# Kernel optimization log

Hardware: AMD Instinct MI355X
Metric: run time of the kernel (lower is better)

## Reference

```python
import jax, jax.numpy as jnp
import numpy as np

B, H, W, C = 32, 56, 56, 192
WS, SS, NH = 7, 3, 6  # window, shift, heads
N = WS * WS
HIDDEN = int(C * 4.0)
TABLE = (2 * WS - 1) * (2 * WS - 1)  # 169
EPS = 1e-5

# Relative position index, faithful to the source (meshgrid default 'xy',
# and the source multiplies BOTH coord channels by (2*ws-1), so indices can
# exceed the table size; gather uses clip like jnp.take's jit behavior).
_coords = np.stack(np.meshgrid(np.arange(WS), np.arange(WS))).reshape(2, -1)
_rel = (_coords[:, :, None] - _coords[:, None, :]).transpose(1, 2, 0)
_rel = (_rel + WS - 1) * (2 * WS - 1)
REL_IDX = jnp.asarray(_rel.sum(-1))  # [N, N]

# Shift attention mask (static), labels regions then marks cross-region pairs.
_m = np.zeros((H, W))
_cnt = 0
for hs in [slice(0, -WS), slice(-WS, -SS), slice(-SS, None)]:
    for ws_ in [slice(0, -WS), slice(-WS, -SS), slice(-SS, None)]:
        _m[hs, ws_] = _cnt
        _cnt += 1
_mw = _m.reshape(H // WS, WS, W // WS, WS).transpose(0, 2, 1, 3).reshape(-1, N)
ATTN_MASK = jnp.asarray((_mw[:, None, :] != _mw[:, :, None]).astype(np.float32))  # [nW, N, N]
NW = ATTN_MASK.shape[0]


def layer_norm(x, g, b):
    mu = jnp.mean(x, axis=-1, keepdims=True)
    xc = x - mu
    var = jnp.mean(xc * xc, axis=-1, keepdims=True)
    return xc * jax.lax.rsqrt(var + EPS) * g + b


def window_partition(x):  # [B,H,W,C] -> [B*nW, N, C]
    x = x.reshape(B, H // WS, WS, W // WS, WS, C).transpose(0, 1, 3, 2, 4, 5)
    return x.reshape(-1, N, C)


def window_reverse(w):  # [B*nW, N, C] -> [B,H,W,C]
    x = w.reshape(B, H // WS, W // WS, WS, WS, C).transpose(0, 1, 3, 2, 4, 5)
    return x.reshape(B, H, W, C)


def setup_inputs() -> dict:
    key = jax.random.key(0)
    ks = jax.random.split(key, 16)
    s = lambda fan_in: 1.0 / np.sqrt(fan_in)
    return {
        "x": jax.random.normal(ks[0], (B, H * W, C), jnp.float32),
        "norm1_g": jnp.ones((C,), jnp.float32),
        "norm1_b": jnp.zeros((C,), jnp.float32),
        "qkv_w": jax.random.normal(ks[1], (C, 3 * C), jnp.float32) * s(C),
        "qkv_b": jnp.zeros((3 * C,), jnp.float32),
        "rel_table": jax.random.normal(ks[2], (TABLE, NH), jnp.float32) * 0.02,
        "proj_w": jax.random.normal(ks[3], (C, C), jnp.float32) * s(C),
        "proj_b": jnp.zeros((C,), jnp.float32),
        "norm2_g": jnp.ones((C,), jnp.float32),
        "norm2_b": jnp.zeros((C,), jnp.float32),
        "fc1_w": jax.random.normal(ks[4], (C, HIDDEN), jnp.float32) * s(C),
        "fc1_b": jnp.zeros((HIDDEN,), jnp.float32),
        "fc2_w": jax.random.normal(ks[5], (HIDDEN, C), jnp.float32) * s(HIDDEN),
        "fc2_b": jnp.zeros((C,), jnp.float32),
    }


def reference(x, norm1_g, norm1_b, qkv_w, qkv_b, rel_table, proj_w, proj_b,
              norm2_g, norm2_b, fc1_w, fc1_b, fc2_w, fc2_b):
    shortcut = x
    h = layer_norm(x, norm1_g, norm1_b).reshape(B, H, W, C)
    # cyclic shift
    h = jnp.roll(h, shift=(-SS, -SS), axis=(1, 2))
    xw = window_partition(h)  # [B*nW, N, C]

    # window attention
    qkv = xw @ qkv_w + qkv_b  # [B*nW, N, 3C]
    q, k, v = jnp.split(qkv, 3, axis=-1)
    hd = C // NH
    q = q.reshape(-1, N, NH, hd).transpose(0, 2, 1, 3) * (hd ** -0.5)
    k = k.reshape(-1, N, NH, hd).transpose(0, 2, 1, 3)
    v = v.reshape(-1, N, NH, hd).transpose(0, 2, 1, 3)
    attn = jnp.einsum("whnd,whmd->whnm", q, k)  # [B*nW, NH, N, N]
    bias = jnp.take(rel_table, REL_IDX, axis=0, mode="clip")  # [N,N,NH]
    attn = attn + bias.transpose(2, 0, 1)[None]
    attn = attn.reshape(B, NW, NH, N, N) + ATTN_MASK[None, :, None] * -100.0
    attn = jax.nn.softmax(attn.reshape(-1, NH, N, N), axis=-1)
    o = jnp.einsum("whnm,whmd->whnd", attn, v)
    o = o.transpose(0, 2, 1, 3).reshape(-1, N, C)
    o = o @ proj_w + proj_b

    h = window_reverse(o)
    h = jnp.roll(h, shift=(SS, SS), axis=(1, 2)).reshape(B, H * W, C)
    x = shortcut + h
    # MLP
    m = layer_norm(x, norm2_g, norm2_b)
    m = jax.nn.gelu(m @ fc1_w + fc1_b, approximate=False) @ fc2_w + fc2_b
    return x + m
```

## Files before the change

### kernel.cpp

```cpp
#include <hip/hip_runtime.h>
#include <hip/hip_bf16.h>


using f32x4  = __attribute__((ext_vector_type(4))) float;
using short8 = __attribute__((ext_vector_type(8))) short;
typedef unsigned short ushort_t;

__device__ __forceinline__ ushort_t f2bf(float f) {
    __hip_bfloat16 h = __float2bfloat16(f);
    return __builtin_bit_cast(ushort_t, h);
}
__device__ __forceinline__ f32x4 mfma16(short8 a, short8 b, f32x4 c) {
    return __builtin_amdgcn_mfma_f32_16x16x32_bf16(a, b, c, 0, 0, 0);
}
__device__ __forceinline__ float fast_gelu(float h) {
    float hh = h * h;
    float p  = __builtin_fmaf(hh, 0.044715f, 1.0f);
    float z  = h * (-1.5957691216057308f);
    float em = __expf(p * z);
    return h * __builtin_amdgcn_rcpf(1.0f + em);
}

#define CC 192

#define OFF_QKVT   0
#define OFF_PROJT  221184
#define OFF_FC1T   294912
#define OFF_FC2T   589824
#define OFF_BIAS   884736
#define OFF_MASK   942592
#define OFF_BMT    1557504
#define OFF_QG     7848960
#define OFF_KG     46384128
#define OFF_VG     84919296
#define WS_NEED    123454464
#define PREP_SMALL 610438
#define PREP_BIG   2183302

__global__ void prep_kernel(const float* __restrict__ qkv_w, const float* __restrict__ proj_w,
                            const float* __restrict__ fc1_w, const float* __restrict__ fc2_w,
                            const float* __restrict__ rel_table,
                            ushort_t* __restrict__ qkvT, ushort_t* __restrict__ projT,
                            ushort_t* __restrict__ fc1T, ushort_t* __restrict__ fc2T,
                            float* __restrict__ biasT, float* __restrict__ maskT,
                            float* __restrict__ bmT, int full) {
    int idx = blockIdx.x * 256 + threadIdx.x;
    if (idx < 110592) { int n = idx / 192, k = idx % 192; qkvT[idx] = f2bf(qkv_w[k * 576 + n]); return; }
    idx -= 110592;
    if (idx < 36864) { int n = idx / 192, k = idx % 192; projT[idx] = f2bf(proj_w[k * 192 + n]); return; }
    idx -= 36864;
    if (idx < 147456) { int n = idx / 192, k = idx % 192; fc1T[idx] = f2bf(fc1_w[k * 768 + n]); return; }
    idx -= 147456;
    if (idx < 147456) { int n = idx / 768, k = idx % 768; fc2T[idx] = f2bf(fc2_w[k * 192 + n]); return; }
    idx -= 147456;
    if (idx < 14406) {
        int h = idx / 2401; int rest = idx % 2401; int a = rest / 49, b = rest % 49;
        int d = 13 * ((a % 7) - (b % 7) + (a / 7) - (b / 7) + 12);
        if (d > 168) d = 168;
        biasT[idx] = rel_table[d * 6 + h];
        return;
    }
    idx -= 14406;
    if (idx < 153664) {
        int w = idx / 2401; int rest = idx % 2401; int a = rest / 49, b = rest % 49;
        int wy = w / 8, wx = w % 8;
        int ya = wy * 7 + a / 7, xa = wx * 7 + a % 7;
        int yb = wy * 7 + b / 7, xb = wx * 7 + b % 7;
        int lya = ya < 49 ? 0 : (ya < 53 ? 1 : 2);
        int lxa = xa < 49 ? 0 : (xa < 53 ? 1 : 2);
        int lyb = yb < 49 ? 0 : (yb < 53 ? 1 : 2);
        int lxb = xb < 49 ? 0 : (xb < 53 ? 1 : 2);
        maskT[idx] = ((lya * 3 + lxa) != (lyb * 3 + lxb)) ? -100.0f : 0.0f;
        return;
    }
    idx -= 153664;
    if (full && idx < 1572864) {
        int wi = idx / 24576; int r2 = idx % 24576;
        int h = r2 / 4096; int r3 = r2 % 4096;
        int col = r3 / 64, row = r3 % 64;
        float v = -1e30f;
        if (row < 49 && col < 49) {
            int d = 13 * ((row % 7) - (col % 7) + (row / 7) - (col / 7) + 12);
            if (d > 168) d = 168;
            float bias = rel_table[d * 6 + h];
            int wy = wi / 8, wx = wi % 8;
            int ya = wy * 7 + row / 7, xa = wx * 7 + row % 7;
            int yb = wy * 7 + col / 7, xb = wx * 7 + col % 7;
            int lya = ya < 49 ? 0 : (ya < 53 ? 1 : 2);
            int lxa = xa < 49 ? 0 : (xa < 53 ? 1 : 2);
            int lyb = yb < 49 ? 0 : (yb < 53 ? 1 : 2);
            int lxb = xb < 49 ? 0 : (xb < 53 ? 1 : 2);
            float mask = ((lya * 3 + lxa) != (lyb * 3 + lxb)) ? -100.0f : 0.0f;
            v = bias + mask;
        }
        bmT[idx] = v;
        return;
    }
}

__global__ __launch_bounds__(256, 3) void lnqkv_kernel(
    const float* __restrict__ x, const float* __restrict__ n1g, const float* __restrict__ n1b,
    const ushort_t* __restrict__ qkvT, const float* __restrict__ qkv_b,
    ushort_t* __restrict__ qg, ushort_t* __restrict__ kg, ushort_t* __restrict__ vg) {
    __shared__ ushort_t xln [64 * 200];
    __shared__ ushort_t qkvs[64 * 200];
    const int tid = threadIdx.x;
    const int wave = tid >> 6, lane = tid & 63;
    const int ln16 = lane & 15, sub = lane >> 4;
    const int t0 = blockIdx.x * 64;
    const f32x4 zero4 = {0.f, 0.f, 0.f, 0.f};

    {
        float g0 = n1g[lane], g1 = n1g[lane + 64], g2 = n1g[lane + 128];
        float bb0 = n1b[lane], bb1 = n1b[lane + 64], bb2 = n1b[lane + 128];
        for (int rb = 0; rb < 4; ++rb) {
            int row0 = wave * 16 + rb * 4;
            float v0[4], v1[4], v2[4], s[4], q[4];
            #pragma unroll
            for (int j = 0; j < 4; ++j) {
                const float* xr = x + (size_t)(t0 + row0 + j) * CC;
                v0[j] = xr[lane]; v1[j] = xr[lane + 64]; v2[j] = xr[lane + 128];
            }
            #pragma unroll
            for (int j = 0; j < 4; ++j) {
                s[j] = v0[j] + v1[j] + v2[j];
                q[j] = v0[j] * v0[j] + v1[j] * v1[j] + v2[j] * v2[j];
            }
            #pragma unroll
            for (int m = 32; m; m >>= 1) {
                #pragma unroll
                for (int j = 0; j < 4; ++j) { s[j] += __shfl_xor(s[j], m); q[j] += __shfl_xor(q[j], m); }
            }
            #pragma unroll
            for (int j = 0; j < 4; ++j) {
                float mu = s[j] * (1.0f / 192.0f);
                float var = q[j] * (1.0f / 192.0f) - mu * mu;
                float rs = rsqrtf(var + 1e-5f);
                int row = row0 + j;
                xln[row * 200 + lane]       = f2bf((v0[j] - mu) * rs * g0 + bb0);
                xln[row * 200 + lane + 64]  = f2bf((v1[j] - mu) * rs * g1 + bb1);
                xln[row * 200 + lane + 128] = f2bf((v2[j] - mu) * rs * g2 + bb2);
            }
        }
    }
    __syncthreads();

    ushort_t* dsts[3] = {qg, kg, vg};
    for (int v = 0; v < 3; ++v) {
        f32x4 acc[4][3];
        #pragma unroll
        for (int m = 0; m < 4; ++m)
            #pragma unroll
            for (int n = 0; n < 3; ++n) acc[m][n] = zero4;
        for (int kk = 0; kk < 6; ++kk) {
            short8 a[4];
            #pragma unroll
            for (int m = 0; m < 4; ++m)
                a[m] = *(const short8*)(xln + (m * 16 + ln16) * 200 + kk * 32 + 8 * sub);
            #pragma unroll
            for (int n = 0; n < 3; ++n) {
                short8 b = *(const short8*)(qkvT + (size_t)(v * 192 + (wave * 3 + n) * 16 + ln16) * 192 + kk * 32 + 8 * sub);
                #pragma unroll
                for (int m = 0; m < 4; ++m) acc[m][n] = mfma16(a[m], b, acc[m][n]);
            }
        }
        #pragma unroll
        for (int n = 0; n < 3; ++n) {
            int col = (wave * 3 + n) * 16 + ln16;
            float bv = qkv_b[v * 192 + col];
            #pragma unroll
            for (int m = 0; m < 4; ++m)
                #pragma unroll
                for (int r = 0; r < 4; ++r) {
                    int row = m * 16 + 4 * sub + r;
                    float val = acc[m][n][r] + bv;
                    if (v == 0) val *= 0.17677669529663689f;
                    qkvs[row * 200 + col] = f2bf(val);
                }
        }
        __syncthreads();
        ushort_t* dst = dsts[v];
        for (int i = tid; i < 1536; i += 256) {
            int row = i / 24, c = i % 24;
            short8 vv = *(const short8*)(qkvs + row * 200 + c * 8);
            *(short8*)(dst + (size_t)(t0 + row) * 192 + c * 8) = vv;
        }
        __syncthreads();
    }
}

__global__ __launch_bounds__(256, 4) void attnwin_kernel(
    const float* __restrict__ x, const float* __restrict__ proj_b,
    const ushort_t* __restrict__ qg, const ushort_t* __restrict__ kg,
    const ushort_t* __restrict__ vg, const ushort_t* __restrict__ projT,
    const float* __restrict__ bmT, float* __restrict__ out) {
    __shared__ ushort_t vt[192 * 72];
    __shared__ ushort_t PO[4][16 * 72];
    const int tid = threadIdx.x;
    const int wave = tid >> 6, lane = tid & 63;
    const int ln16 = lane & 15, sub = lane >> 4;
    const int win = blockIdx.x;
    const int b = win >> 6, wi = win & 63;
    const int wy = wi >> 3, wx = wi & 7;
    const f32x4 zero4 = {0.f, 0.f, 0.f, 0.f};

    {
        int j = tid & 63;
        int jj = j < 49 ? j : 48;
        int y  = wy * 7 + jj / 7 + 3; if (y >= 56) y -= 56;
        int xx = wx * 7 + jj % 7 + 3; if (xx >= 56) xx -= 56;
        size_t tokV = (size_t)(b * 3136 + y * 56 + xx);
        const bool valid = j < 49;
        #pragma unroll
        for (int pass = 0; pass < 6; ++pass) {
            int c8 = pass * 32 + (tid >> 6) * 8;
            if (valid) {
                short8 vv = *(const short8*)(vg + tokV * 192 + c8);
                #pragma unroll
                for (int q = 0; q < 8; ++q) vt[(c8 + q) * 72 + j] = ((ushort_t*)&vv)[q];
            } else {
                #pragma unroll
                for (int q = 0; q < 8; ++q) vt[(c8 + q) * 72 + j] = 0;
            }
        }
    }

    size_t tokA;
    {
        int j = wave * 16 + ln16; if (j > 48) j = 48;
        int y  = wy * 7 + j / 7 + 3; if (y >= 56) y -= 56;
        int xx = wx * 7 + j % 7 + 3; if (xx >= 56) xx -= 56;
        tokA = (size_t)(b * 3136 + y * 56 + xx);
    }
    size_t tokB[4];
    #pragma unroll
    for (int n = 0; n < 4; ++n) {
        int j = n * 16 + ln16; if (j > 48) j = 48;
        int y  = wy * 7 + j / 7 + 3; if (y >= 56) y -= 56;
        int xx = wx * 7 + j % 7 + 3; if (xx >= 56) xx -= 56;
        tokB[n] = (size_t)(b * 3136 + y * 56 + xx);
    }

    f32x4 accP[12];
    #pragma unroll
    for (int n = 0; n < 12; ++n) accP[n] = zero4;

    ushort_t* Pw = PO[wave];
    const float* bmw = bmT + (size_t)wi * 24576 + (size_t)(wave * 16 + 4 * sub);
    __syncthreads();

    for (int h = 0; h < 6; ++h) {
        short8 qf = *(const short8*)(qg + tokA * 192 + h * 32 + 8 * sub);
        f32x4 s4[4];
        #pragma unroll
        for (int n = 0; n < 4; ++n) {
            short8 kf = *(const short8*)(kg + tokB[n] * 192 + h * 32 + 8 * sub);
            s4[n] = mfma16(qf, kf, zero4);
        }
        #pragma unroll
        for (int n = 0; n < 4; ++n) {
            int col = n * 16 + ln16;
            f32x4 bv = *(const f32x4*)(bmw + h * 4096 + col * 64);
            #pragma unroll
            for (int r = 0; r < 4; ++r) s4[n][r] += bv[r];
        }
        #pragma unroll
        for (int r = 0; r < 4; ++r) {
            float mx = fmaxf(fmaxf(s4[0][r], s4[1][r]), fmaxf(s4[2][r], s4[3][r]));
            mx = fmaxf(mx, __shfl_xor(mx, 1, 16));
            mx = fmaxf(mx, __shfl_xor(mx, 2, 16));
            mx = fmaxf(mx, __shfl_xor(mx, 4, 16));
            mx = fmaxf(mx, __shfl_xor(mx, 8, 16));
            float e0 = __expf(s4[0][r] - mx), e1 = __expf(s4[1][r] - mx);
            float e2 = __expf(s4[2][r] - mx), e3 = __expf(s4[3][r] - mx);
            float sm = e0 + e1 + e2 + e3;
            sm += __shfl_xor(sm, 1, 16);
            sm += __shfl_xor(sm, 2, 16);
            sm += __shfl_xor(sm, 4, 16);
            sm += __shfl_xor(sm, 8, 16);
            float inv = 1.0f / sm;
            int rl = 4 * sub + r;
            Pw[rl * 72 +      ln16] = f2bf(e0 * inv);
            Pw[rl * 72 + 16 + ln16] = f2bf(e1 * inv);
            Pw[rl * 72 + 32 + ln16] = f2bf(e2 * inv);
            Pw[rl * 72 + 48 + ln16] = f2bf(e3 * inv);
        }
        short8 ap0 = *(const short8*)(Pw + ln16 * 72 + 8 * sub);
        short8 ap1 = *(const short8*)(Pw + ln16 * 72 + 32 + 8 * sub);
        f32x4 o2[2]; o2[0] = zero4; o2[1] = zero4;
        #pragma unroll
        for (int n2 = 0; n2 < 2; ++n2) {
            short8 bv0 = *(const short8*)(vt + (h * 32 + n2 * 16 + ln16) * 72 + 8 * sub);
            short8 bv1 = *(const short8*)(vt + (h * 32 + n2 * 16 + ln16) * 72 + 32 + 8 * sub);
            o2[n2] = mfma16(ap0, bv0, o2[n2]);
            o2[n2] = mfma16(ap1, bv1, o2[n2]);
        }
        #pragma unroll
        for (int n2 = 0; n2 < 2; ++n2)
            #pragma unroll
            for (int r = 0; r < 4; ++r)
                Pw[(4 * sub + r) * 72 + n2 * 16 + ln16] = f2bf(o2[n2][r]);
        {
            short8 ao = *(const short8*)(Pw + ln16 * 72 + 8 * sub);
            #pragma unroll
            for (int n = 0; n < 12; ++n) {
                short8 bp = *(const short8*)(projT + (size_t)(n * 16 + ln16) * 192 + h * 32 + 8 * sub);
                accP[n] = mfma16(ao, bp, accP[n]);
            }
        }
    }

    #pragma unroll
    for (int n = 0; n < 12; ++n) {
        int col = n * 16 + ln16;
        float pb = proj_b[col];
        #pragma unroll
        for (int r = 0; r < 4; ++r) {
            int row = wave * 16 + 4 * sub + r;
            if (row < 49) {
                int y  = wy * 7 + row / 7 + 3; if (y >= 56) y -= 56;
                int xx = wx * 7 + row % 7 + 3; if (xx >= 56) xx -= 56;
                size_t g = (size_t)(b * 3136 + y * 56 + xx) * CC;
                out[g + col] = accP[n][r] + pb + x[g + col];
            }
        }
    }
}

__global__ __launch_bounds__(256, 3) void attn_kernel(
    const float* __restrict__ x, const float* __restrict__ n1g, const float* __restrict__ n1b,
    const float* __restrict__ qkv_b, const float* __restrict__ proj_b,
    const ushort_t* __restrict__ qkvT, const ushort_t* __restrict__ projT,
    const float* __restrict__ biasT, const float* __restrict__ maskT,
    float* __restrict__ out) {
    __shared__ ushort_t xln[64 * 200];
    __shared__ ushort_t qo [64 * 40];
    __shared__ ushort_t kl [64 * 40];
    __shared__ ushort_t vt [32 * 72];
    __shared__ ushort_t Pl [64 * 72];
    const int tid = threadIdx.x;
    const int wave = tid >> 6, lane = tid & 63;
    const int ln16 = lane & 15, sub = lane >> 4;
    const int w = blockIdx.x;
    const int batch = w >> 6, wi = w & 63;
    const int wy = wi >> 3, wx = wi & 7;
    const f32x4 zero4 = {0.f, 0.f, 0.f, 0.f};

    for (int rr = 0; rr < 16; ++rr) {
        int row = wave * 16 + rr;
        if (row < 49) {
            int ty = row / 7, tx = row % 7;
            int y  = wy * 7 + ty + 3; if (y >= 56) y -= 56;
            int xx = wx * 7 + tx + 3; if (xx >= 56) xx -= 56;
            const float* xr = x + (size_t)(batch * 3136 + y * 56 + xx) * CC;
            float v0 = xr[lane], v1 = xr[lane + 64], v2 = xr[lane + 128];
            float s = v0 + v1 + v2;
            #pragma unroll
            for (int m = 32; m; m >>= 1) s += __shfl_xor(s, m);
            float mu = s * (1.0f / 192.0f);
            float d0 = v0 - mu, d1 = v1 - mu, d2 = v2 - mu;
            float q = d0 * d0 + d1 * d1 + d2 * d2;
            #pragma unroll
            for (int m = 32; m; m >>= 1) q += __shfl_xor(q, m);
            float rs = rsqrtf(q * (1.0f / 192.0f) + 1e-5f);
            xln[row * 200 + lane]       = f2bf(d0 * rs * n1g[lane]       + n1b[lane]);
            xln[row * 200 + lane + 64]  = f2bf(d1 * rs * n1g[lane + 64]  + n1b[lane + 64]);
            xln[row * 200 + lane + 128] = f2bf(d2 * rs * n1g[lane + 128] + n1b[lane + 128]);
        } else {
            xln[row * 200 + lane] = 0; xln[row * 200 + lane + 64] = 0; xln[row * 200 + lane + 128] = 0;
        }
    }

    f32x4 accP[12];
    #pragma unroll
    for (int n = 0; n < 12; ++n) accP[n] = zero4;
    const float scale = 0.17677669529663689f;
    const float* mptr = maskT + wi * 2401;

    for (int h = 0; h < 6; ++h) {
        f32x4 acc6[6];
        #pragma unroll
        for (int n = 0; n < 6; ++n) acc6[n] = zero4;
        const int cb0 = h * 32;
        for (int kk = 0; kk < 6; ++kk) {
            short8 a = *(const short8*)(xln + (wave * 16 + ln16) * 200 + kk * 32 + 8 * sub);
            #pragma unroll
            for (int n = 0; n < 6; ++n) {
                int colbase = (n >> 1) * 192 + cb0 + (n & 1) * 16;
                short8 b = *(const short8*)(qkvT + (size_t)(colbase + ln16) * 192 + kk * 32 + 8 * sub);
                acc6[n] = mfma16(a, b, acc6[n]);
            }
        }
        #pragma unroll
        for (int n = 0; n < 6; ++n) {
            int colbase = (n >> 1) * 192 + cb0 + (n & 1) * 16;
            float bv = qkv_b[colbase + ln16];
            int dim = (n & 1) * 16 + ln16;
            #pragma unroll
            for (int r = 0; r < 4; ++r) {
                int row = wave * 16 + 4 * sub + r;
                ushort_t hv = f2bf(acc6[n][r] + bv);
                if (n < 2)      qo[row * 40 + dim] = hv;
                else if (n < 4) kl[row * 40 + dim] = hv;
                else            vt[dim * 72 + row] = hv;
            }
        }
        __syncthreads();

        f32x4 s4[4];
        {
            short8 aq = *(const short8*)(qo + (wave * 16 + ln16) * 40 + 8 * sub);
            #pragma unroll
            for (int n = 0; n < 4; ++n) {
                short8 bk = *(const short8*)(kl + (n * 16 + ln16) * 40 + 8 * sub);
                s4[n] = mfma16(aq, bk, zero4);
            }
        }
        const float* bptr = biasT + h * 2401;
        #pragma unroll
        for (int n = 0; n < 4; ++n) {
            int col = n * 16 + ln16;
            #pragma unroll
            for (int r = 0; r < 4; ++r) {
                int row = wave * 16 + 4 * sub + r;
                s4[n][r] = (row < 49 && col < 49)
                    ? s4[n][r] * scale + bptr[row * 49 + col] + mptr[row * 49 + col]
                    : -1e30f;
            }
        }
        #pragma unroll
        for (int r = 0; r < 4; ++r) {
            float mx = fmaxf(fmaxf(s4[0][r], s4[1][r]), fmaxf(s4[2][r], s4[3][r]));
            mx = fmaxf(mx, __shfl_xor(mx, 1, 16));
            mx = fmaxf(mx, __shfl_xor(mx, 2, 16));
            mx = fmaxf(mx, __shfl_xor(mx, 4, 16));
            mx = fmaxf(mx, __shfl_xor(mx, 8, 16));
            float e0 = __expf(s4[0][r] - mx), e1 = __expf(s4[1][r] - mx);
            float e2 = __expf(s4[2][r] - mx), e3 = __expf(s4[3][r] - mx);
            float sm = e0 + e1 + e2 + e3;
            sm += __shfl_xor(sm, 1, 16);
            sm += __shfl_xor(sm, 2, 16);
            sm += __shfl_xor(sm, 4, 16);
            sm += __shfl_xor(sm, 8, 16);
            float inv = 1.0f / sm;
            int row = wave * 16 + 4 * sub + r;
            Pl[row * 72 +      ln16] = f2bf(e0 * inv);
            Pl[row * 72 + 16 + ln16] = f2bf(e1 * inv);
            Pl[row * 72 + 32 + ln16] = f2bf(e2 * inv);
            Pl[row * 72 + 48 + ln16] = f2bf(e3 * inv);
        }
        f32x4 o2[2]; o2[0] = zero4; o2[1] = zero4;
        #pragma unroll
        for (int ks = 0; ks < 2; ++ks) {
            short8 ap = *(const short8*)(Pl + (wave * 16 + ln16) * 72 + ks * 32 + 8 * sub);
            #pragma unroll
            for (int n2 = 0; n2 < 2; ++n2) {
                short8 bv = *(const short8*)(vt + (n2 * 16 + ln16) * 72 + ks * 32 + 8 * sub);
                o2[n2] = mfma16(ap, bv, o2[n2]);
            }
        }
        #pragma unroll
        for (int n2 = 0; n2 < 2; ++n2)
            #pragma unroll
            for (int r = 0; r < 4; ++r) {
                int row = wave * 16 + 4 * sub + r;
                qo[row * 40 + n2 * 16 + ln16] = f2bf(o2[n2][r]);
            }
        {
            short8 ao = *(const short8*)(qo + (wave * 16 + ln16) * 40 + 8 * sub);
            #pragma unroll
            for (int n = 0; n < 12; ++n) {
                short8 bp = *(const short8*)(projT + (size_t)(n * 16 + ln16) * 192 + h * 32 + 8 * sub);
                accP[n] = mfma16(ao, bp, accP[n]);
            }
        }
        __syncthreads();
    }

    #pragma unroll
    for (int n = 0; n < 12; ++n) {
        int col = n * 16 + ln16;
        float pb = proj_b[col];
        #pragma unroll
        for (int r = 0; r < 4; ++r) {
            int row = wave * 16 + 4 * sub + r;
            if (row < 49) {
                int ty = row / 7, tx = row % 7;
                int y  = wy * 7 + ty + 3; if (y >= 56) y -= 56;
                int xx = wx * 7 + tx + 3; if (xx >= 56) xx -= 56;
                size_t g = (size_t)(batch * 3136 + y * 56 + xx) * CC;
                out[g + col] = accP[n][r] + pb + x[g + col];
            }
        }
    }
}

__global__ __launch_bounds__(256, 3) void mlp5_kernel(
    float* __restrict__ out, const float* __restrict__ n2g, const float* __restrict__ n2b,
    const float* __restrict__ fc1_b, const float* __restrict__ fc2_b,
    const ushort_t* __restrict__ fc1T, const ushort_t* __restrict__ fc2T) {
    __shared__ ushort_t smem[2][64 * 200];
    ushort_t* aln  = smem[0];
    ushort_t* hidc = smem[1];
    float* fout = (float*)&smem[0][0];
    const int tid = threadIdx.x;
    const int wave = tid >> 6, lane = tid & 63;
    const int ln16 = lane & 15, sub = lane >> 4;
    const size_t t0 = (size_t)blockIdx.x * 64;
    const f32x4 zero4 = {0.f, 0.f, 0.f, 0.f};

    short8 b1p[3];
    #pragma unroll
    for (int n = 0; n < 3; ++n)
        b1p[n] = *(const short8*)(fc1T + (size_t)(wave * 48 + n * 16 + ln16) * 192 + 8 * sub);

    {
        float g0 = n2g[lane], g1 = n2g[lane + 64], g2 = n2g[lane + 128];
        float bb0 = n2b[lane], bb1 = n2b[lane + 64], bb2 = n2b[lane + 128];
        for (int rb = 0; rb < 4; ++rb) {
            int row0 = wave * 16 + rb * 4;
            float v0[4], v1[4], v2[4], s[4], q[4];
            #pragma unroll
            for (int j = 0; j < 4; ++j) {
                const float* xr = out + (t0 + row0 + j) * CC;
                v0[j] = xr[lane]; v1[j] = xr[lane + 64]; v2[j] = xr[lane + 128];
            }
            #pragma unroll
            for (int j = 0; j < 4; ++j) {
                s[j] = v0[j] + v1[j] + v2[j];
                q[j] = v0[j] * v0[j] + v1[j] * v1[j] + v2[j] * v2[j];
            }
            #pragma unroll
            for (int m = 32; m; m >>= 1) {
                #pragma unroll
                for (int j = 0; j < 4; ++j) { s[j] += __shfl_xor(s[j], m); q[j] += __shfl_xor(q[j], m); }
            }
            #pragma unroll
            for (int j = 0; j < 4; ++j) {
                float mu = s[j] * (1.0f / 192.0f);
                float var = q[j] * (1.0f / 192.0f) - mu * mu;
                float rs = rsqrtf(var + 1e-5f);
                int row = row0 + j;
                aln[row * 200 + lane]       = f2bf((v0[j] - mu) * rs * g0 + bb0);
                aln[row * 200 + lane + 64]  = f2bf((v1[j] - mu) * rs * g1 + bb1);
                aln[row * 200 + lane + 128] = f2bf((v2[j] - mu) * rs * g2 + bb2);
            }
        }
    }
    __syncthreads();

    f32x4 accO[4][3];
    #pragma unroll
    for (int m = 0; m < 4; ++m)
        #pragma unroll
        for (int n = 0; n < 3; ++n) accO[m][n] = zero4;

    for (int c = 0; c < 4; ++c) {
        f32x4 acc1[4][3];
        #pragma unroll
        for (int m = 0; m < 4; ++m)
            #pragma unroll
            for (int n = 0; n < 3; ++n) acc1[m][n] = zero4;
        #pragma unroll
        for (int kk = 0; kk < 6; ++kk) {
            short8 a[4];
            #pragma unroll
            for (int m = 0; m < 4; ++m)
                a[m] = *(const short8*)(aln + (m * 16 + ln16) * 200 + kk * 32 + 8 * sub);
            short8 bb[3];
            if (kk == 0) {
                bb[0] = b1p[0]; bb[1] = b1p[1]; bb[2] = b1p[2];
            } else {
                #pragma unroll
                for (int n = 0; n < 3; ++n)
                    bb[n] = *(const short8*)(fc1T + (size_t)(c * 192 + wave * 48 + n * 16 + ln16) * 192 + kk * 32 + 8 * sub);
            }
            __builtin_amdgcn_s_setprio(1);
            #pragma unroll
            for (int n = 0; n < 3; ++n)
                #pragma unroll
                for (int m = 0; m < 4; ++m) acc1[m][n] = mfma16(a[m], bb[n], acc1[m][n]);
            __builtin_amdgcn_s_setprio(0);
        }
        short8 b2p[3];
        #pragma unroll
        for (int n = 0; n < 3; ++n)
            b2p[n] = *(const short8*)(fc2T + (size_t)(wave * 48 + n * 16 + ln16) * 768 + c * 192 + 8 * sub);
        if (c < 3) {
            #pragma unroll
            for (int n = 0; n < 3; ++n)
                b1p[n] = *(const short8*)(fc1T + (size_t)((c + 1) * 192 + wave * 48 + n * 16 + ln16) * 192 + 8 * sub);
        }
        #pragma unroll
        for (int n = 0; n < 3; ++n) {
            int cl = wave * 48 + n * 16 + ln16;
            float fb = fc1_b[c * 192 + cl];
            #pragma unroll
            for (int m = 0; m < 4; ++m)
                #pragma unroll
                for (int r = 0; r < 4; ++r) {
                    float hv = acc1[m][n][r] + fb;
                    hidc[(m * 16 + 4 * sub + r) * 200 + cl] = f2bf(fast_gelu(hv));
                }
        }
        __syncthreads();
        #pragma unroll
        for (int kk = 0; kk < 6; ++kk) {
            short8 a[4];
            #pragma unroll
            for (int m = 0; m < 4; ++m)
                a[m] = *(const short8*)(hidc + (m * 16 + ln16) * 200 + kk * 32 + 8 * sub);
            short8 bb[3];
            if (kk == 0) {
                bb[0] = b2p[0]; bb[1] = b2p[1]; bb[2] = b2p[2];
            } else {
                #pragma unroll
                for (int n = 0; n < 3; ++n)
                    bb[n] = *(const short8*)(fc2T + (size_t)(wave * 48 + n * 16 + ln16) * 768 + c * 192 + kk * 32 + 8 * sub);
            }
            __builtin_amdgcn_s_setprio(1);
            #pragma unroll
            for (int n = 0; n < 3; ++n)
                #pragma unroll
                for (int m = 0; m < 4; ++m) accO[m][n] = mfma16(a[m], bb[n], accO[m][n]);
            __builtin_amdgcn_s_setprio(0);
        }
        __syncthreads();
    }

    #pragma unroll
    for (int n = 0; n < 3; ++n) {
        int col = wave * 48 + n * 16 + ln16;
        float fb = fc2_b[col];
        #pragma unroll
        for (int m = 0; m < 4; ++m)
            #pragma unroll
            for (int r = 0; r < 4; ++r)
                fout[(m * 16 + 4 * sub + r) * 196 + col] = accO[m][n][r] + fb;
    }
    __syncthreads();
    for (int i = tid; i < 3072; i += 256) {
        int row = i / 48, c4 = (i % 48) * 4;
        f32x4 sv = *(const f32x4*)(fout + row * 196 + c4);
        float* op = out + (t0 + row) * CC + c4;
        f32x4 ov = *(const f32x4*)op;
        #pragma unroll
        for (int q = 0; q < 4; ++q) ov[q] += sv[q];
        *(f32x4*)op = ov;
    }
}

extern "C" void kernel_launch(void* const* d_in, const int* in_sizes, int n_in,
                              void* d_out, int out_size, void* d_ws, size_t ws_size,
                              hipStream_t stream) {
    const float* x      = (const float*)d_in[0];
    const float* n1g    = (const float*)d_in[1];
    const float* n1b    = (const float*)d_in[2];
    const float* qkv_w  = (const float*)d_in[3];
    const float* qkv_b  = (const float*)d_in[4];
    const float* rel_t  = (const float*)d_in[5];
    const float* proj_w = (const float*)d_in[6];
    const float* proj_b = (const float*)d_in[7];
    const float* n2g    = (const float*)d_in[8];
    const float* n2b    = (const float*)d_in[9];
    const float* fc1_w  = (const float*)d_in[10];
    const float* fc1_b  = (const float*)d_in[11];
    const float* fc2_w  = (const float*)d_in[12];
    const float* fc2_b  = (const float*)d_in[13];
    float* out = (float*)d_out;

    char* ws = (char*)d_ws;
    ushort_t* qkvT  = (ushort_t*)(ws + OFF_QKVT);
    ushort_t* projT = (ushort_t*)(ws + OFF_PROJT);
    ushort_t* fc1T  = (ushort_t*)(ws + OFF_FC1T);
    ushort_t* fc2T  = (ushort_t*)(ws + OFF_FC2T);
    float* biasT    = (float*)(ws + OFF_BIAS);
    float* maskT    = (float*)(ws + OFF_MASK);
    float* bmT      = (float*)(ws + OFF_BMT);
    ushort_t* qg    = (ushort_t*)(ws + OFF_QG);
    ushort_t* kg    = (ushort_t*)(ws + OFF_KG);
    ushort_t* vg    = (ushort_t*)(ws + OFF_VG);

    const int big = ws_size >= (size_t)WS_NEED;
    const int prep_total = big ? PREP_BIG : PREP_SMALL;
    prep_kernel<<<(prep_total + 255) / 256, 256, 0, stream>>>(
        qkv_w, proj_w, fc1_w, fc2_w, rel_t, qkvT, projT, fc1T, fc2T, biasT, maskT, bmT, big);

    if (big) {
        lnqkv_kernel<<<1568, 256, 0, stream>>>(x, n1g, n1b, qkvT, qkv_b, qg, kg, vg);
        attnwin_kernel<<<2048, 256, 0, stream>>>(x, proj_b, qg, kg, vg, projT, bmT, out);
    } else {
        attn_kernel<<<2048, 256, 0, stream>>>(x, n1g, n1b, qkv_b, proj_b,
                                              qkvT, projT, biasT, maskT, out);
    }
    mlp5_kernel<<<1568, 256, 0, stream>>>(out, n2g, n2b, fc1_b, fc2_b, fc1T, fc2T);
}
```

Baseline: 438.3 us.

## Shrink MLP tile to 32 rows, prefetch per-head Q/K/bias in window attention

The MLP kernel now processes 32 tokens per block instead of 64, doubling the grid and halving shared memory and accumulator registers so more blocks can be resident. The explicit weight prefetch and setprio scheduling hints are dropped. In the window-attention kernel, the next head's Q, K and bias loads are issued before the current head's softmax, and the head loop is unrolled to hide global-load latency, with launch bounds lowered to 3 blocks per CU. Weight reuse per block falls in the MLP, and the extra prefetch registers may reduce attention occupancy.

Measured after the change: 499.3 us. +13.9%, slower.

```diff
diff --git a/kernel.cpp b/kernel.cpp
--- a/kernel.cpp
+++ b/kernel.cpp
@@ -189,7 +189,7 @@
     }
 }
 
-__global__ __launch_bounds__(256, 4) void attnwin_kernel(
+__global__ __launch_bounds__(256, 3) void attnwin_kernel(
     const float* __restrict__ x, const float* __restrict__ proj_b,
     const ushort_t* __restrict__ qg, const ushort_t* __restrict__ kg,
     const ushort_t* __restrict__ vg, const ushort_t* __restrict__ projT,
@@ -204,6 +204,32 @@
     const int wy = wi >> 3, wx = wi & 7;
     const f32x4 zero4 = {0.f, 0.f, 0.f, 0.f};
 
+    size_t tokA;
+    {
+        int j = wave * 16 + ln16; if (j > 48) j = 48;
+        int y  = wy * 7 + j / 7 + 3; if (y >= 56) y -= 56;
+        int xx = wx * 7 + j % 7 + 3; if (xx >= 56) xx -= 56;
+        tokA = (size_t)(b * 3136 + y * 56 + xx);
+    }
+    size_t tokB[4];
+    #pragma unroll
+    for (int n = 0; n < 4; ++n) {
+        int j = n * 16 + ln16; if (j > 48) j = 48;
+        int y  = wy * 7 + j / 7 + 3; if (y >= 56) y -= 56;
+        int xx = wx * 7 + j % 7 + 3; if (xx >= 56) xx -= 56;
+        tokB[n] = (size_t)(b * 3136 + y * 56 + xx);
+    }
+    const float* bmw = bmT + (size_t)wi * 24576 + (size_t)(wave * 16 + 4 * sub);
+
+    short8 qf = *(const short8*)(qg + tokA * 192 + 8 * sub);
+    short8 kf[4];
+    f32x4  bv[4];
+    #pragma unroll
+    for (int n = 0; n < 4; ++n) {
+        kf[n] = *(const short8*)(kg + tokB[n] * 192 + 8 * sub);
+        bv[n] = *(const f32x4*)(bmw + (n * 16 + ln16) * 64);
+    }
+
     {
         int j = tid & 63;
         int jj = j < 49 ? j : 48;
@@ -225,45 +251,30 @@
         }
     }
 
-    size_t tokA;
-    {
-        int j = wave * 16 + ln16; if (j > 48) j = 48;
-        int y  = wy * 7 + j / 7 + 3; if (y >= 56) y -= 56;
-        int xx = wx * 7 + j % 7 + 3; if (xx >= 56) xx -= 56;
-        tokA = (size_t)(b * 3136 + y * 56 + xx);
-    }
-    size_t tokB[4];
-    #pragma unroll
-    for (int n = 0; n < 4; ++n) {
-        int j = n * 16 + ln16; if (j > 48) j = 48;
-        int y  = wy * 7 + j / 7 + 3; if (y >= 56) y -= 56;
-        int xx = wx * 7 + j % 7 + 3; if (xx >= 56) xx -= 56;
-        tokB[n] = (size_t)(b * 3136 + y * 56 + xx);
-    }
-
     f32x4 accP[12];
     #pragma unroll
     for (int n = 0; n < 12; ++n) accP[n] = zero4;
-
     ushort_t* Pw = PO[wave];
-    const float* bmw = bmT + (size_t)wi * 24576 + (size_t)(wave * 16 + 4 * sub);
     __syncthreads();
 
+    #pragma unroll
     for (int h = 0; h < 6; ++h) {
-        short8 qf = *(const short8*)(qg + tokA * 192 + h * 32 + 8 * sub);
         f32x4 s4[4];
         #pragma unroll
-        for (int n = 0; n < 4; ++n) {
-            short8 kf = *(const short8*)(kg + tokB[n] * 192 + h * 32 + 8 * sub);
-            s4[n] = mfma16(qf, kf, zero4);
-        }
-        #pragma unroll
-        for (int n = 0; n < 4; ++n) {
-            int col = n * 16 + ln16;
-            f32x4 bv = *(const f32x4*)(bmw + h * 4096 + col * 64);
-            #pragma unroll
-            for (int r = 0; r < 4; ++r) s4[n][r] += bv[r];
-        }
+        for (int n = 0; n < 4; ++n) s4[n] = mfma16(qf, kf[n], zero4);
+        short8 qn; short8 kn[4]; f32x4 bn[4];
+        if (h < 5) {
+            qn = *(const short8*)(qg + tokA * 192 + (h + 1) * 32 + 8 * sub);
+            #pragma unroll
+            for (int n = 0; n < 4; ++n) {
+                kn[n] = *(const short8*)(kg + tokB[n] * 192 + (h + 1) * 32 + 8 * sub);
+                bn[n] = *(const f32x4*)(bmw + (h + 1) * 4096 + (n * 16 + ln16) * 64);
+            }
+        }
+        #pragma unroll
+        for (int n = 0; n < 4; ++n)
+            #pragma unroll
+            for (int r = 0; r < 4; ++r) s4[n][r] += bv[n][r];
         #pragma unroll
         for (int r = 0; r < 4; ++r) {
             float mx = fmaxf(fmaxf(s4[0][r], s4[1][r]), fmaxf(s4[2][r], s4[3][r]));
@@ -308,6 +319,11 @@
                 accP[n] = mfma16(ao, bp, accP[n]);
             }
         }
+        if (h < 5) {
+            qf = qn;
+            #pragma unroll
+            for (int n = 0; n < 4; ++n) { kf[n] = kn[n]; bv[n] = bn[n]; }
+        }
     }
 
     #pragma unroll
@@ -495,30 +511,25 @@
     }
 }
 
-__global__ __launch_bounds__(256, 3) void mlp5_kernel(
+__global__ __launch_bounds__(256, 4) void mlp6_kernel(
     float* __restrict__ out, const float* __restrict__ n2g, const float* __restrict__ n2b,
     const float* __restrict__ fc1_b, const float* __restrict__ fc2_b,
     const ushort_t* __restrict__ fc1T, const ushort_t* __restrict__ fc2T) {
-    __shared__ ushort_t smem[2][64 * 200];
+    __shared__ ushort_t smem[2][32 * 200];
     ushort_t* aln  = smem[0];
     ushort_t* hidc = smem[1];
     float* fout = (float*)&smem[0][0];
     const int tid = threadIdx.x;
     const int wave = tid >> 6, lane = tid & 63;
     const int ln16 = lane & 15, sub = lane >> 4;
-    const size_t t0 = (size_t)blockIdx.x * 64;
+    const size_t t0 = (size_t)blockIdx.x * 32;
     const f32x4 zero4 = {0.f, 0.f, 0.f, 0.f};
-
-    short8 b1p[3];
-    #pragma unroll
-    for (int n = 0; n < 3; ++n)
-        b1p[n] = *(const short8*)(fc1T + (size_t)(wave * 48 + n * 16 + ln16) * 192 + 8 * sub);
 
     {
         float g0 = n2g[lane], g1 = n2g[lane + 64], g2 = n2g[lane + 128];
         float bb0 = n2b[lane], bb1 = n2b[lane + 64], bb2 = n2b[lane + 128];
-        for (int rb = 0; rb < 4; ++rb) {
-            int row0 = wave * 16 + rb * 4;
+        for (int rb = 0; rb < 2; ++rb) {
+            int row0 = wave * 8 + rb * 4;
             float v0[4], v1[4], v2[4], s[4], q[4];
             #pragma unroll
             for (int j = 0; j < 4; ++j) {
@@ -549,54 +560,37 @@
     }
     __syncthreads();
 
-    f32x4 accO[4][3];
-    #pragma unroll
-    for (int m = 0; m < 4; ++m)
+    f32x4 accO[2][3];
+    #pragma unroll
+    for (int m = 0; m < 2; ++m)
         #pragma unroll
         for (int n = 0; n < 3; ++n) accO[m][n] = zero4;
 
     for (int c = 0; c < 4; ++c) {
-        f32x4 acc1[4][3];
-        #pragma unroll
-        for (int m = 0; m < 4; ++m)
+        f32x4 acc1[2][3];
+        #pragma unroll
+        for (int m = 0; m < 2; ++m)
             #pragma unroll
             for (int n = 0; n < 3; ++n) acc1[m][n] = zero4;
         #pragma unroll
         for (int kk = 0; kk < 6; ++kk) {
-            short8 a[4];
-            #pragma unroll
-            for (int m = 0; m < 4; ++m)
+            short8 a[2];
+            #pragma unroll
+            for (int m = 0; m < 2; ++m)
                 a[m] = *(const short8*)(aln + (m * 16 + ln16) * 200 + kk * 32 + 8 * sub);
-            short8 bb[3];
-            if (kk == 0) {
-                bb[0] = b1p[0]; bb[1] = b1p[1]; bb[2] = b1p[2];
-            } else {
-                #pragma unroll
-                for (int n = 0; n < 3; ++n)
-                    bb[n] = *(const short8*)(fc1T + (size_t)(c * 192 + wave * 48 + n * 16 + ln16) * 192 + kk * 32 + 8 * sub);
-            }
-            __builtin_amdgcn_s_setprio(1);
-            #pragma unroll
-            for (int n = 0; n < 3; ++n)
-                #pragma unroll
-                for (int m = 0; m < 4; ++m) acc1[m][n] = mfma16(a[m], bb[n], acc1[m][n]);
-            __builtin_amdgcn_s_setprio(0);
-        }
-        short8 b2p[3];
-        #pragma unroll
-        for (int n = 0; n < 3; ++n)
-            b2p[n] = *(const short8*)(fc2T + (size_t)(wave * 48 + n * 16 + ln16) * 768 + c * 192 + 8 * sub);
-        if (c < 3) {
-            #pragma unroll
-            for (int n = 0; n < 3; ++n)
-                b1p[n] = *(const short8*)(fc1T + (size_t)((c + 1) * 192 + wave * 48 + n * 16 + ln16) * 192 + 8 * sub);
+            #pragma unroll
+            for (int n = 0; n < 3; ++n) {
+                short8 bb = *(const short8*)(fc1T + (size_t)(c * 192 + wave * 48 + n * 16 + ln16) * 192 + kk * 32 + 8 * sub);
+                #pragma unroll
+                for (int m = 0; m < 2; ++m) acc1[m][n] = mfma16(a[m], bb, acc1[m][n]);
+            }
         }
         #pragma unroll
         for (int n = 0; n < 3; ++n) {
             int cl = wave * 48 + n * 16 + ln16;
             float fb = fc1_b[c * 192 + cl];
             #pragma unroll
-            for (int m = 0; m < 4; ++m)
+            for (int m = 0; m < 2; ++m)
                 #pragma unroll
                 for (int r = 0; r < 4; ++r) {
                     float hv = acc1[m][n][r] + fb;
@@ -606,24 +600,16 @@
         __syncthreads();
         #pragma unroll
         for (int kk = 0; kk < 6; ++kk) {
-            short8 a[4];
-            #pragma unroll
-            for (int m = 0; m < 4; ++m)
+            short8 a[2];
+            #pragma unroll
+            for (int m = 0; m < 2; ++m)
                 a[m] = *(const short8*)(hidc + (m * 16 + ln16) * 200 + kk * 32 + 8 * sub);
-            short8 bb[3];
-            if (kk == 0) {
-                bb[0] = b2p[0]; bb[1] = b2p[1]; bb[2] = b2p[2];
-            } else {
-                #pragma unroll
-                for (int n = 0; n < 3; ++n)
-                    bb[n] = *(const short8*)(fc2T + (size_t)(wave * 48 + n * 16 + ln16) * 768 + c * 192 + kk * 32 + 8 * sub);
-            }
-            __builtin_amdgcn_s_setprio(1);
-            #pragma unroll
-            for (int n = 0; n < 3; ++n)
-                #pragma unroll
-                for (int m = 0; m < 4; ++m) accO[m][n] = mfma16(a[m], bb[n], accO[m][n]);
-            __builtin_amdgcn_s_setprio(0);
+            #pragma unroll
+            for (int n = 0; n < 3; ++n) {
+                short8 bb = *(const short8*)(fc2T + (size_t)(wave * 48 + n * 16 + ln16) * 768 + c * 192 + kk * 32 + 8 * sub);
+                #pragma unroll
+                for (int m = 0; m < 2; ++m) accO[m][n] = mfma16(a[m], bb, accO[m][n]);
+            }
         }
         __syncthreads();
     }
@@ -633,13 +619,13 @@
         int col = wave * 48 + n * 16 + ln16;
         float fb = fc2_b[col];
         #pragma unroll
-        for (int m = 0; m < 4; ++m)
+        for (int m = 0; m < 2; ++m)
             #pragma unroll
             for (int r = 0; r < 4; ++r)
                 fout[(m * 16 + 4 * sub + r) * 196 + col] = accO[m][n][r] + fb;
     }
     __syncthreads();
-    for (int i = tid; i < 3072; i += 256) {
+    for (int i = tid; i < 1536; i += 256) {
         int row = i / 48, c4 = (i % 48) * 4;
         f32x4 sv = *(const f32x4*)(fout + row * 196 + c4);
         float* op = out + (t0 + row) * CC + c4;
@@ -693,5 +679,5 @@
         attn_kernel<<<2048, 256, 0, stream>>>(x, n1g, n1b, qkv_b, proj_b,
                                               qkvT, projT, biasT, maskT, out);
     }
-    mlp5_kernel<<<1568, 256, 0, stream>>>(out, n2g, n2b, fc1_b, fc2_b, fc1T, fc2T);
-}
+    mlp6_kernel<<<3136, 256, 0, stream>>>(out, n2g, n2b, fc1_b, fc2_b, fc1T, fc2T);
+}
```

## Fuse MLP into windowed attention kernel and prefetch next head operands

Applied to the files above, without the earlier changes.

Merges LayerNorm2, FC1+GELU and FC2 into the per-window attention kernel, so the attention output stays in registers/LDS rather than being reread by a separate MLP kernel. The head loop also prefetches the next head's q, k and bias fragments to hide global load latency. In exchange, the MLP now runs on 64-row window tiles holding only 49 valid tokens, which wastes matrix work. Shared memory grows and occupancy bounds drop from 4 to 3 blocks.

After: 436.5 us. Within noise of the previous version (-0.4%).

```diff
diff --git a/kernel.cpp b/kernel.cpp
--- a/kernel.cpp
+++ b/kernel.cpp
@@ -189,13 +189,22 @@
     }
 }
 
-__global__ __launch_bounds__(256, 4) void attnwin_kernel(
+__global__ __launch_bounds__(256, 3) void attnmlp_kernel(
     const float* __restrict__ x, const float* __restrict__ proj_b,
     const ushort_t* __restrict__ qg, const ushort_t* __restrict__ kg,
     const ushort_t* __restrict__ vg, const ushort_t* __restrict__ projT,
-    const float* __restrict__ bmT, float* __restrict__ out) {
-    __shared__ ushort_t vt[192 * 72];
-    __shared__ ushort_t PO[4][16 * 72];
+    const float* __restrict__ bmT,
+    const float* __restrict__ n2g, const float* __restrict__ n2b,
+    const float* __restrict__ fc1_b, const float* __restrict__ fc2_b,
+    const ushort_t* __restrict__ fc1T, const ushort_t* __restrict__ fc2T,
+    float* __restrict__ out) {
+    __shared__ __align__(16) char smem[51200];
+    ushort_t* vt   = (ushort_t*)smem;
+    ushort_t* PO   = (ushort_t*)(smem + 27648);
+    ushort_t* aln  = (ushort_t*)smem;
+    ushort_t* hidc = (ushort_t*)(smem + 25600);
+    float*    fout = (float*)smem;
+
     const int tid = threadIdx.x;
     const int wave = tid >> 6, lane = tid & 63;
     const int ln16 = lane & 15, sub = lane >> 4;
@@ -204,6 +213,32 @@
     const int wy = wi >> 3, wx = wi & 7;
     const f32x4 zero4 = {0.f, 0.f, 0.f, 0.f};
 
+    size_t tokA;
+    {
+        int j = wave * 16 + ln16; if (j > 48) j = 48;
+        int y  = wy * 7 + j / 7 + 3; if (y >= 56) y -= 56;
+        int xx = wx * 7 + j % 7 + 3; if (xx >= 56) xx -= 56;
+        tokA = (size_t)(b * 3136 + y * 56 + xx);
+    }
+    size_t tokB[4];
+    #pragma unroll
+    for (int n = 0; n < 4; ++n) {
+        int j = n * 16 + ln16; if (j > 48) j = 48;
+        int y  = wy * 7 + j / 7 + 3; if (y >= 56) y -= 56;
+        int xx = wx * 7 + j % 7 + 3; if (xx >= 56) xx -= 56;
+        tokB[n] = (size_t)(b * 3136 + y * 56 + xx);
+    }
+    const float* bmw = bmT + (size_t)wi * 24576 + (size_t)(wave * 16 + 4 * sub);
+
+    short8 qf = *(const short8*)(qg + tokA * 192 + 8 * sub);
+    short8 kf[4];
+    f32x4  bv[4];
+    #pragma unroll
+    for (int n = 0; n < 4; ++n) {
+        kf[n] = *(const short8*)(kg + tokB[n] * 192 + 8 * sub);
+        bv[n] = *(const f32x4*)(bmw + (n * 16 + ln16) * 64);
+    }
+
     {
         int j = tid & 63;
         int jj = j < 49 ? j : 48;
@@ -225,45 +260,30 @@
         }
     }
 
-    size_t tokA;
-    {
-        int j = wave * 16 + ln16; if (j > 48) j = 48;
-        int y  = wy * 7 + j / 7 + 3; if (y >= 56) y -= 56;
-        int xx = wx * 7 + j % 7 + 3; if (xx >= 56) xx -= 56;
-        tokA = (size_t)(b * 3136 + y * 56 + xx);
-    }
-    size_t tokB[4];
-    #pragma unroll
-    for (int n = 0; n < 4; ++n) {
-        int j = n * 16 + ln16; if (j > 48) j = 48;
-        int y  = wy * 7 + j / 7 + 3; if (y >= 56) y -= 56;
-        int xx = wx * 7 + j % 7 + 3; if (xx >= 56) xx -= 56;
-        tokB[n] = (size_t)(b * 3136 + y * 56 + xx);
-    }
-
     f32x4 accP[12];
     #pragma unroll
     for (int n = 0; n < 12; ++n) accP[n] = zero4;
-
-    ushort_t* Pw = PO[wave];
-    const float* bmw = bmT + (size_t)wi * 24576 + (size_t)(wave * 16 + 4 * sub);
+    ushort_t* Pw = PO + wave * (16 * 72);
     __syncthreads();
 
+    #pragma unroll
     for (int h = 0; h < 6; ++h) {
-        short8 qf = *(const short8*)(qg + tokA * 192 + h * 32 + 8 * sub);
         f32x4 s4[4];
         #pragma unroll
-        for (int n = 0; n < 4; ++n) {
-            short8 kf = *(const short8*)(kg + tokB[n] * 192 + h * 32 + 8 * sub);
-            s4[n] = mfma16(qf, kf, zero4);
-        }
-        #pragma unroll
-        for (int n = 0; n < 4; ++n) {
-            int col = n * 16 + ln16;
-            f32x4 bv = *(const f32x4*)(bmw + h * 4096 + col * 64);
-            #pragma unroll
-            for (int r = 0; r < 4; ++r) s4[n][r] += bv[r];
-        }
+        for (int n = 0; n < 4; ++n) s4[n] = mfma16(qf, kf[n], zero4);
+        short8 qn; short8 kn[4]; f32x4 bn[4];
+        if (h < 5) {
+            qn = *(const short8*)(qg + tokA * 192 + (h + 1) * 32 + 8 * sub);
+            #pragma unroll
+            for (int n = 0; n < 4; ++n) {
+                kn[n] = *(const short8*)(kg + tokB[n] * 192 + (h + 1) * 32 + 8 * sub);
+                bn[n] = *(const f32x4*)(bmw + (h + 1) * 4096 + (n * 16 + ln16) * 64);
+            }
+        }
+        #pragma unroll
+        for (int n = 0; n < 4; ++n)
+            #pragma unroll
+            for (int r = 0; r < 4; ++r) s4[n][r] += bv[n][r];
         #pragma unroll
         for (int r = 0; r < 4; ++r) {
             float mx = fmaxf(fmaxf(s4[0][r], s4[1][r]), fmaxf(s4[2][r], s4[3][r]));
@@ -308,6 +328,11 @@
                 accP[n] = mfma16(ao, bp, accP[n]);
             }
         }
+        if (h < 5) {
+            qf = qn;
+            #pragma unroll
+            for (int n = 0; n < 4; ++n) { kf[n] = kn[n]; bv[n] = bn[n]; }
+        }
     }
 
     #pragma unroll
@@ -317,13 +342,166 @@
         #pragma unroll
         for (int r = 0; r < 4; ++r) {
             int row = wave * 16 + 4 * sub + r;
+            float v = accP[n][r] + pb;
             if (row < 49) {
                 int y  = wy * 7 + row / 7 + 3; if (y >= 56) y -= 56;
                 int xx = wx * 7 + row % 7 + 3; if (xx >= 56) xx -= 56;
                 size_t g = (size_t)(b * 3136 + y * 56 + xx) * CC;
-                out[g + col] = accP[n][r] + pb + x[g + col];
-            }
-        }
+                v += x[g + col];
+                out[g + col] = v;
+            }
+            accP[n][r] = v;
+        }
+    }
+    __threadfence_block();
+
+    float mu4[4], rs4[4];
+    {
+        float s[4], qs[4];
+        #pragma unroll
+        for (int r = 0; r < 4; ++r) { s[r] = 0.f; qs[r] = 0.f; }
+        #pragma unroll
+        for (int n = 0; n < 12; ++n)
+            #pragma unroll
+            for (int r = 0; r < 4; ++r) {
+                float v = accP[n][r];
+                s[r] += v; qs[r] += v * v;
+            }
+        #pragma unroll
+        for (int m = 1; m < 16; m <<= 1) {
+            #pragma unroll
+            for (int r = 0; r < 4; ++r) {
+                s[r]  += __shfl_xor(s[r],  m, 16);
+                qs[r] += __shfl_xor(qs[r], m, 16);
+            }
+        }
+        #pragma unroll
+        for (int r = 0; r < 4; ++r) {
+            float mu = s[r] * (1.0f / 192.0f);
+            float var = qs[r] * (1.0f / 192.0f) - mu * mu;
+            mu4[r] = mu;
+            rs4[r] = rsqrtf(var + 1e-5f);
+        }
+    }
+    __syncthreads();
+
+    short8 b1p[3];
+    #pragma unroll
+    for (int n = 0; n < 3; ++n)
+        b1p[n] = *(const short8*)(fc1T + (size_t)(wave * 48 + n * 16 + ln16) * 192 + 8 * sub);
+
+    #pragma unroll
+    for (int n = 0; n < 12; ++n) {
+        int col = n * 16 + ln16;
+        float g = n2g[col], bb = n2b[col];
+        #pragma unroll
+        for (int r = 0; r < 4; ++r) {
+            int row = wave * 16 + 4 * sub + r;
+            aln[row * 200 + col] = f2bf((accP[n][r] - mu4[r]) * rs4[r] * g + bb);
+        }
+    }
+    __syncthreads();
+
+    f32x4 accO[4][3];
+    #pragma unroll
+    for (int m = 0; m < 4; ++m)
+        #pragma unroll
+        for (int n = 0; n < 3; ++n) accO[m][n] = zero4;
+
+    for (int c = 0; c < 4; ++c) {
+        f32x4 acc1[4][3];
+        #pragma unroll
+        for (int m = 0; m < 4; ++m)
+            #pragma unroll
+            for (int n = 0; n < 3; ++n) acc1[m][n] = zero4;
+        #pragma unroll
+        for (int kk = 0; kk < 6; ++kk) {
+            short8 a[4];
+            #pragma unroll
+            for (int m = 0; m < 4; ++m)
+                a[m] = *(const short8*)(aln + (m * 16 + ln16) * 200 + kk * 32 + 8 * sub);
+            short8 bb[3];
+            if (kk == 0) {
+                bb[0] = b1p[0]; bb[1] = b1p[1]; bb[2] = b1p[2];
+            } else {
+                #pragma unroll
+                for (int n = 0; n < 3; ++n)
+                    bb[n] = *(const short8*)(fc1T + (size_t)(c * 192 + wave * 48 + n * 16 + ln16) * 192 + kk * 32 + 8 * sub);
+            }
+            __builtin_amdgcn_s_setprio(1);
+            #pragma unroll
+            for (int n = 0; n < 3; ++n)
+                #pragma unroll
+                for (int m = 0; m < 4; ++m) acc1[m][n] = mfma16(a[m], bb[n], acc1[m][n]);
+            __builtin_amdgcn_s_setprio(0);
+        }
+        short8 b2p[3];
+        #pragma unroll
+        for (int n = 0; n < 3; ++n)
+            b2p[n] = *(const short8*)(fc2T + (size_t)(wave * 48 + n * 16 + ln16) * 768 + c * 192 + 8 * sub);
+        if (c < 3) {
+            #pragma unroll
+            for (int n = 0; n < 3; ++n)
+                b1p[n] = *(const short8*)(fc1T + (size_t)((c + 1) * 192 + wave * 48 + n * 16 + ln16) * 192 + 8 * sub);
+        }
+        #pragma unroll
+        for (int n = 0; n < 3; ++n) {
+            int cl = wave * 48 + n * 16 + ln16;
+            float fb = fc1_b[c * 192 + cl];
+            #pragma unroll
+            for (int m = 0; m < 4; ++m)
+                #pragma unroll
+                for (int r = 0; r < 4; ++r) {
+                    float hv = acc1[m][n][r] + fb;
+                    hidc[(m * 16 + 4 * sub + r) * 200 + cl] = f2bf(fast_gelu(hv));
+                }
+        }
+        __syncthreads();
+        #pragma unroll
+        for (int kk = 0; kk < 6; ++kk) {
+            short8 a[4];
+            #pragma unroll
+            for (int m = 0; m < 4; ++m)
+                a[m] = *(const short8*)(hidc + (m * 16 + ln16) * 200 + kk * 32 + 8 * sub);
+            short8 bb[3];
+            if (kk == 0) {
+                bb[0] = b2p[0]; bb[1] = b2p[1]; bb[2] = b2p[2];
+            } else {
+                #pragma unroll
+                for (int n = 0; n < 3; ++n)
+                    bb[n] = *(const short8*)(fc2T + (size_t)(wave * 48 + n * 16 + ln16) * 768 + c * 192 + kk * 32 + 8 * sub);
+            }
+            __builtin_amdgcn_s_setprio(1);
+            #pragma unroll
+            for (int n = 0; n < 3; ++n)
+                #pragma unroll
+                for (int m = 0; m < 4; ++m) accO[m][n] = mfma16(a[m], bb[n], accO[m][n]);
+            __builtin_amdgcn_s_setprio(0);
+        }
+        __syncthreads();
+    }
+
+    #pragma unroll
+    for (int n = 0; n < 3; ++n) {
+        int col = wave * 48 + n * 16 + ln16;
+        float fb = fc2_b[col];
+        #pragma unroll
+        for (int m = 0; m < 4; ++m)
+            #pragma unroll
+            for (int r = 0; r < 4; ++r)
+                fout[(m * 16 + 4 * sub + r) * 196 + col] = accO[m][n][r] + fb;
+    }
+    __syncthreads();
+    for (int i = tid; i < 2352; i += 256) {
+        int row = i / 48, c4 = (i % 48) * 4;
+        int y  = wy * 7 + row / 7 + 3; if (y >= 56) y -= 56;
+        int xx = wx * 7 + row % 7 + 3; if (xx >= 56) xx -= 56;
+        float* op = out + (size_t)(b * 3136 + y * 56 + xx) * CC + c4;
+        f32x4 sv = *(const f32x4*)(fout + row * 196 + c4);
+        f32x4 ov = *(const f32x4*)op;
+        #pragma unroll
+        for (int q = 0; q < 4; ++q) ov[q] += sv[q];
+        *(f32x4*)op = ov;
     }
 }
 
@@ -688,10 +866,11 @@
 
     if (big) {
         lnqkv_kernel<<<1568, 256, 0, stream>>>(x, n1g, n1b, qkvT, qkv_b, qg, kg, vg);
-        attnwin_kernel<<<2048, 256, 0, stream>>>(x, proj_b, qg, kg, vg, projT, bmT, out);
+        attnmlp_kernel<<<2048, 256, 0, stream>>>(x, proj_b, qg, kg, vg, projT, bmT,
+                                                 n2g, n2b, fc1_b, fc2_b, fc1T, fc2T, out);
     } else {
         attn_kernel<<<2048, 256, 0, stream>>>(x, n1g, n1b, qkv_b, proj_b,
                                               qkvT, projT, biasT, maskT, out);
-    }
-    mlp5_kernel<<<1568, 256, 0, stream>>>(out, n2g, n2b, fc1_b, fc2_b, fc1T, fc2T);
+        mlp5_kernel<<<1568, 256, 0, stream>>>(out, n2g, n2b, fc1_b, fc2_b, fc1T, fc2T);
+    }
 }
```
